# Kernel tuning notes

Measured on AMD Instinct MI355X. Metric: run time of the kernel, lower is better.

## Reference

```python
import jax, jax.numpy as jnp
import numpy as np

N = 50000      # nodes
E = 800000     # edges (avg degree 16)
IN = 128       # in_channels
HID = 64       # hidden_channels
OUT = 64       # out_channels
H = 2          # attention heads
EDIM = 16      # edge feature dim
NEG_SLOPE = 0.2


def setup_inputs() -> dict:
    key = jax.random.key(0)
    ks = jax.random.split(key, 16)
    p = lambda k, shape: (jax.random.normal(k, shape, jnp.float32) * 0.1)
    return {
        'x': jax.random.normal(ks[0], (N, IN), jnp.float32),
        'edge_index': jax.random.randint(ks[1], (2, E), 0, N, dtype=jnp.int64),
        'edge_attr': jax.random.normal(ks[2], (E, EDIM), jnp.float32),
        # GAT layer 1 (in=IN -> HID, heads=H, concat=False, edge_dim=EDIM)
        'W1': p(ks[3], (IN, H * HID)),
        'We1': p(ks[4], (EDIM, H * HID)),
        'as1': p(ks[5], (H, HID)),
        'ad1': p(ks[6], (H, HID)),
        'ae1': p(ks[7], (H, HID)),
        'b1': jnp.zeros((HID,), jnp.float32),
        # GAT layer 2 (in=HID -> OUT)
        'W2': p(ks[8], (HID, H * OUT)),
        'We2': p(ks[9], (EDIM, H * OUT)),
        'as2': p(ks[10], (H, OUT)),
        'ad2': p(ks[11], (H, OUT)),
        'ae2': p(ks[12], (H, OUT)),
        'b2': jnp.zeros((OUT,), jnp.float32),
    }


def _add_self_loops(edge_index, edge_attr, n):
    # PyG GATConv default: add_self_loops=True, fill_value='mean' ->
    # self-loop edge_attr[i] = mean of edge_attr over edges with dst == i.
    src, dst = edge_index[0], edge_index[1]
    attr_sum = jax.ops.segment_sum(edge_attr, dst, num_segments=n)          # [N, EDIM]
    cnt = jax.ops.segment_sum(jnp.ones((edge_attr.shape[0],), edge_attr.dtype), dst, num_segments=n)
    loop_attr = attr_sum / jnp.maximum(cnt, 1.0)[:, None]
    loop = jnp.arange(n, dtype=src.dtype)
    return jnp.concatenate([src, loop]), jnp.concatenate([dst, loop]), jnp.concatenate([edge_attr, loop_attr], axis=0)


def gat_layer(x, edge_index, edge_attr, W, We, att_src, att_dst, att_edge, bias, heads, out_ch):
    """PyG GATConv with edge_dim, concat=False (mean over heads)."""
    n = x.shape[0]
    src, dst, ea = _add_self_loops(edge_index, edge_attr, n)
    h = (x @ W).reshape(n, heads, out_ch)                 # [N, H, C]
    e = (ea @ We).reshape(-1, heads, out_ch)              # [E', H, C]
    a_src = jnp.sum(h * att_src, axis=-1)                 # [N, H]
    a_dst = jnp.sum(h * att_dst, axis=-1)                 # [N, H]
    a_edge = jnp.sum(e * att_edge, axis=-1)               # [E', H]
    alpha = jax.nn.leaky_relu(a_src[src] + a_dst[dst] + a_edge, NEG_SLOPE)  # [E', H]
    # segment softmax over destination node (self-loops guarantee nonempty segments)
    amax = jax.ops.segment_max(alpha, dst, num_segments=n)
    ex = jnp.exp(alpha - amax[dst])
    denom = jax.ops.segment_sum(ex, dst, num_segments=n)
    attn = ex / (denom[dst] + 1e-16)                      # [E', H]
    msg = h[src] * attn[:, :, None]                       # [E', H, C]
    out = jax.ops.segment_sum(msg, dst, num_segments=n)   # [N, H, C]
    return jnp.mean(out, axis=1) + bias, attn


def reference(x, edge_index, edge_attr, W1, We1, as1, ad1, ae1, b1, W2, We2, as2, ad2, ae2, b2):
    h1, _attn1 = gat_layer(x, edge_index, edge_attr, W1, We1, as1, ad1, ae1, b1, H, HID)
    h1 = jax.nn.relu(h1)
    h2, _attn2 = gat_layer(h1, edge_index, edge_attr, W2, We2, as2, ad2, ae2, b2, H, OUT)
    return h2
```

## Files before the change

kernel.cpp:

```cpp
#include <hip/hip_runtime.h>

#define N_NODES 50000
#define N_EDGES 800000
#define EDIM 16
#define NEG_SLOPE 0.2f

typedef _Float16 f16x8 __attribute__((ext_vector_type(8)));
typedef _Float16 f16x4 __attribute__((ext_vector_type(4)));
typedef _Float16 f16x2 __attribute__((ext_vector_type(2)));
typedef float f32x4 __attribute__((ext_vector_type(4)));

__global__ void count_rank_kernel(const int* __restrict__ ei, int* __restrict__ cnt,
                                  int* __restrict__ rank) {
    int e = blockIdx.x * blockDim.x + threadIdx.x;
    if (e < N_EDGES) rank[e] = atomicAdd(&cnt[ei[N_EDGES + e]], 1);
}

__global__ void scan_block_kernel(const int* __restrict__ in, int* __restrict__ excl,
                                  int* __restrict__ bsums, int n) {
    __shared__ int sh[256];
    int tid = threadIdx.x;
    int gid = blockIdx.x * 256 + tid;
    int v = (gid < n) ? in[gid] : 0;
    sh[tid] = v;
    __syncthreads();
    for (int off = 1; off < 256; off <<= 1) {
        int t = (tid >= off) ? sh[tid - off] : 0;
        __syncthreads();
        sh[tid] += t;
        __syncthreads();
    }
    if (gid < n) excl[gid] = sh[tid] - v;
    if (bsums != nullptr && tid == 255) bsums[blockIdx.x] = sh[tid];
}

__global__ void scan_add_kernel(const int* __restrict__ excl, const int* __restrict__ bs2,
                                int* __restrict__ csr_off, int n, int total) {
    int gid = blockIdx.x * 256 + threadIdx.x;
    if (gid < n) csr_off[gid] = excl[gid] + bs2[gid >> 8];
    if (gid == 0) csr_off[n] = total;
}

__global__ void we2_kernel(const float* __restrict__ We1, const float* __restrict__ ae1,
                           const float* __restrict__ We2, const float* __restrict__ ae2,
                           float* __restrict__ w_e) {
    int idx = threadIdx.x;
    if (idx >= 64) return;
    const float* We = (idx < 32) ? We1 : We2;
    const float* ae = (idx < 32) ? ae1 : ae2;
    int i = idx & 31;
    int h = i >> 4, d = i & 15;
    float s = 0.f;
    for (int c = 0; c < 64; ++c) s += We[d * 128 + h * 64 + c] * ae[h * 64 + c];
    w_e[idx] = s;
}

__global__ void scatter_pack_kernel(const int* __restrict__ ei, const float* __restrict__ edge_attr,
                                    const float* __restrict__ w_e, const int* __restrict__ csr_off,
                                    const int* __restrict__ rank, uint4* __restrict__ recs) {
    int e = blockIdx.x * blockDim.x + threadIdx.x;
    if (e >= N_EDGES) return;
    int s = ei[e];
    int d = ei[N_EDGES + e];
    const float* ea = edge_attr + (size_t)e * 16;
    float4 dd = make_float4(0.f, 0.f, 0.f, 0.f);
#pragma unroll
    for (int q = 0; q < 4; ++q) {
        float4 v = *reinterpret_cast<const float4*>(ea + q * 4);
        float4 wa = *reinterpret_cast<const float4*>(w_e + q * 4);
        float4 wb = *reinterpret_cast<const float4*>(w_e + 16 + q * 4);
        float4 wc = *reinterpret_cast<const float4*>(w_e + 32 + q * 4);
        float4 wd = *reinterpret_cast<const float4*>(w_e + 48 + q * 4);
        dd.x += v.x * wa.x + v.y * wa.y + v.z * wa.z + v.w * wa.w;
        dd.y += v.x * wb.x + v.y * wb.y + v.z * wb.z + v.w * wb.w;
        dd.z += v.x * wc.x + v.y * wc.y + v.z * wc.z + v.w * wc.w;
        dd.w += v.x * wd.x + v.y * wd.y + v.z * wd.z + v.w * wd.w;
    }
    f16x2 p1 = {(_Float16)dd.x, (_Float16)dd.y};
    f16x2 p2 = {(_Float16)dd.z, (_Float16)dd.w};
    int pos = csr_off[d] + rank[e];
    uint4 rec;
    rec.x = (unsigned)s;
    rec.y = __builtin_bit_cast(unsigned int, p1);
    rec.z = __builtin_bit_cast(unsigned int, p2);
    rec.w = 0u;
    recs[pos] = rec;
}

template <int K, bool F16IN>
__global__ __launch_bounds__(256) void gemm_att_kernel(const void* __restrict__ Xv,
                                                       const float* __restrict__ W,
                                                       const float* __restrict__ as_,
                                                       const float* __restrict__ ad_,
                                                       _Float16* __restrict__ H16,
                                                       float2* __restrict__ a_src,
                                                       float2* __restrict__ a_dst, int M) {
    constexpr int NCH = K / 32;
    __shared__ _Float16 wlds[8 * NCH * 64 * 8];
    const int tid = threadIdx.x;

    for (int idx = tid; idx < K * 128; idx += 256) {
        int k = idx >> 7, c = idx & 127;
        int ct = c >> 4, cl = c & 15;
        int chunk = k >> 5, grp = (k >> 3) & 3, j = k & 7;
        wlds[(((ct * NCH) + chunk) * 64 + (grp * 16 + cl)) * 8 + j] = (_Float16)W[idx];
    }
    __syncthreads();

    const int wv = tid >> 6, lane = tid & 63;
    const int lcol = lane & 15, lgrp = lane >> 4;
    const int row0 = blockIdx.x * 64 + wv * 16;
    int arow = row0 + lcol;
    if (arow >= M) arow = M - 1;

    f32x4 acc[8];
#pragma unroll
    for (int ct = 0; ct < 8; ++ct) acc[ct] = (f32x4){0.f, 0.f, 0.f, 0.f};

#pragma unroll
    for (int chunk = 0; chunk < NCH; ++chunk) {
        f16x8 afrag;
        if constexpr (F16IN) {
            const _Float16* aptr = (const _Float16*)Xv + (size_t)arow * K + lgrp * 8;
            afrag = *reinterpret_cast<const f16x8*>(aptr + chunk * 32);
        } else {
            const float* aptr = (const float*)Xv + (size_t)arow * K + lgrp * 8;
            float4 va = *reinterpret_cast<const float4*>(aptr + chunk * 32);
            float4 vb = *reinterpret_cast<const float4*>(aptr + chunk * 32 + 4);
            afrag = (f16x8){(_Float16)va.x, (_Float16)va.y, (_Float16)va.z, (_Float16)va.w,
                            (_Float16)vb.x, (_Float16)vb.y, (_Float16)vb.z, (_Float16)vb.w};
        }
#pragma unroll
        for (int ct = 0; ct < 8; ++ct) {
            f16x8 bfrag = *reinterpret_cast<const f16x8*>(&wlds[((ct * NCH + chunk) * 64 + lane) * 8]);
            acc[ct] = __builtin_amdgcn_mfma_f32_16x16x32_f16(afrag, bfrag, acc[ct], 0, 0, 0);
        }
    }

    float asv[8], adv[8];
#pragma unroll
    for (int ct = 0; ct < 8; ++ct) {
        asv[ct] = as_[ct * 16 + lcol];
        adv[ct] = ad_[ct * 16 + lcol];
    }

#pragma unroll
    for (int r = 0; r < 4; ++r) {
        int grow = row0 + lgrp * 4 + r;
        float s0 = 0.f, s1 = 0.f, d0 = 0.f, d1 = 0.f;
#pragma unroll
        for (int ct = 0; ct < 8; ++ct) {
            float v = acc[ct][r];
            if (grow < M) H16[(size_t)grow * 128 + ct * 16 + lcol] = (_Float16)v;
            if (ct < 4) { s0 += v * asv[ct]; d0 += v * adv[ct]; }
            else        { s1 += v * asv[ct]; d1 += v * adv[ct]; }
        }
#pragma unroll
        for (int m = 1; m < 16; m <<= 1) {
            s0 += __shfl_xor(s0, m);
            s1 += __shfl_xor(s1, m);
            d0 += __shfl_xor(d0, m);
            d1 += __shfl_xor(d1, m);
        }
        if (lcol == 0 && grow < M) {
            a_src[grow] = make_float2(s0, s1);
            a_dst[grow] = make_float2(d0, d1);
        }
    }
}

#define AGG_STAGE(PREG, II)                                                        \
    do {                                                                           \
        int sl_ = 2 * (II) + sub;                                                  \
        float e0b_ = __shfl(ex0, sl_);                                             \
        float e1b_ = __shfl(ex1, sl_);                                             \
        float exu_ = h1sel ? e1b_ : e0b_;                                          \
        int svn_ = __shfl(sv, (sl_ + 4) & 63);                                     \
        acc0 = fmaf(exu_, (float)PREG.x, acc0);                                    \
        acc1 = fmaf(exu_, (float)PREG.y, acc1);                                    \
        acc2 = fmaf(exu_, (float)PREG.z, acc2);                                    \
        acc3 = fmaf(exu_, (float)PREG.w, acc3);                                    \
        PREG = *reinterpret_cast<const f16x4*>(hb + ((size_t)(unsigned)svn_ << 8)); \
    } while (0)

__global__ void aggregate_kernel(const int* __restrict__ csr_off, const uint4* __restrict__ recs,
                                 const float2* __restrict__ a_src, const float2* __restrict__ a_dst,
                                 const _Float16* __restrict__ H16, const float* __restrict__ bias,
                                 float* __restrict__ out32, _Float16* __restrict__ out16,
                                 int layer, int do_relu) {
    int wid = (blockIdx.x * blockDim.x + threadIdx.x) >> 6;
    int lane = threadIdx.x & 63;
    if (wid >= N_NODES) return;
    const int n = wid;
    const int q = lane & 31;
    const int sub = lane >> 5;
    const bool h1sel = q >= 16;
    const char* hb = reinterpret_cast<const char*>(H16) + q * 8;

    float2 adn = a_dst[n];
    float2 asn = a_src[n];
    int b = csr_off[n], e = csr_off[n + 1];

    float acc0 = 0.f, acc1 = 0.f, acc2 = 0.f, acc3 = 0.f;
    float den0 = 0.f, den1 = 0.f;
    float sae0 = 0.f, sae1 = 0.f;

    for (int base = b; base < e; base += 64) {
        int j = base + lane;
        bool act = j < e;
        int sv = n;
        float ex0 = 0.f, ex1 = 0.f;
        if (act) {
            uint4 rec = recs[j];
            sv = (int)rec.x;
            unsigned aeu = layer ? rec.z : rec.y;
            f16x2 aev = __builtin_bit_cast(f16x2, aeu);
            float ael0 = (float)aev.x, ael1 = (float)aev.y;
            sae0 += ael0;
            sae1 += ael1;
            float2 asv = a_src[sv];
            float q0 = asv.x + adn.x + ael0;
            float q1 = asv.y + adn.y + ael1;
            q0 = (q0 > 0.f) ? q0 : NEG_SLOPE * q0;
            q1 = (q1 > 0.f) ? q1 : NEG_SLOPE * q1;
            ex0 = __expf(q0);
            ex1 = __expf(q1);
        }
        float d0 = ex0, d1 = ex1;
#pragma unroll
        for (int m = 32; m; m >>= 1) {
            d0 += __shfl_xor(d0, m);
            d1 += __shfl_xor(d1, m);
        }
        den0 += d0;
        den1 += d1;

        int m = e - base;
        if (m > 64) m = 64;
        int nit = (m + 1) >> 1;
        f16x4 pA, pB;
        int s0_ = __shfl(sv, sub);
        pA = *reinterpret_cast<const f16x4*>(hb + ((size_t)(unsigned)s0_ << 8));
        int s1_ = __shfl(sv, 2 + sub);
        pB = *reinterpret_cast<const f16x4*>(hb + ((size_t)(unsigned)s1_ << 8));
        for (int i = 0; i < nit; i += 2) {
            AGG_STAGE(pA, i);
            AGG_STAGE(pB, i + 1);
        }
    }

    acc0 += __shfl_xor(acc0, 32);
    acc1 += __shfl_xor(acc1, 32);
    acc2 += __shfl_xor(acc2, 32);
    acc3 += __shfl_xor(acc3, 32);

#pragma unroll
    for (int m = 32; m; m >>= 1) {
        sae0 += __shfl_xor(sae0, m);
        sae1 += __shfl_xor(sae1, m);
    }
    int deg = e - b;
    float invd = (deg > 0) ? (1.f / (float)deg) : 0.f;
    float l0 = asn.x + adn.x + sae0 * invd;
    float l1 = asn.y + adn.y + sae1 * invd;
    l0 = (l0 > 0.f) ? l0 : NEG_SLOPE * l0;
    l1 = (l1 > 0.f) ? l1 : NEG_SLOPE * l1;
    float exs0 = __expf(l0), exs1 = __expf(l1);
    den0 += exs0;
    den1 += exs1;
    float exsu = h1sel ? exs1 : exs0;
    f16x4 hs = *reinterpret_cast<const f16x4*>(hb + ((size_t)(unsigned)n << 8));
    acc0 = fmaf(exsu, (float)hs.x, acc0);
    acc1 = fmaf(exsu, (float)hs.y, acc1);
    acc2 = fmaf(exsu, (float)hs.z, acc2);
    acc3 = fmaf(exsu, (float)hs.w, acc3);

    float invden = 1.f / ((h1sel ? den1 : den0) + 1e-16f);
    float r0 = acc0 * invden;
    float r1 = acc1 * invden;
    float r2 = acc2 * invden;
    float r3 = acc3 * invden;
    float t0 = __shfl_xor(r0, 16);
    float t1 = __shfl_xor(r1, 16);
    float t2 = __shfl_xor(r2, 16);
    float t3 = __shfl_xor(r3, 16);
    if (lane < 16) {
        float4 bv = *reinterpret_cast<const float4*>(bias + q * 4);
        float o0 = 0.5f * (r0 + t0) + bv.x;
        float o1 = 0.5f * (r1 + t1) + bv.y;
        float o2 = 0.5f * (r2 + t2) + bv.z;
        float o3 = 0.5f * (r3 + t3) + bv.w;
        if (do_relu) {
            o0 = fmaxf(o0, 0.f); o1 = fmaxf(o1, 0.f);
            o2 = fmaxf(o2, 0.f); o3 = fmaxf(o3, 0.f);
        }
        if (out32) {
            float4 ov = {o0, o1, o2, o3};
            *reinterpret_cast<float4*>(out32 + (size_t)n * 64 + q * 4) = ov;
        }
        if (out16) {
            f16x4 ov16 = {(_Float16)o0, (_Float16)o1, (_Float16)o2, (_Float16)o3};
            *reinterpret_cast<f16x4*>(out16 + (size_t)n * 64 + q * 4) = ov16;
        }
    }
}

extern "C" void kernel_launch(void* const* d_in, const int* in_sizes, int n_in,
                              void* d_out, int out_size, void* d_ws, size_t ws_size,
                              hipStream_t stream) {
    const float* x = (const float*)d_in[0];
    const int* ei = (const int*)d_in[1];
    const float* edge_attr = (const float*)d_in[2];
    const float* W1 = (const float*)d_in[3];
    const float* We1 = (const float*)d_in[4];
    const float* as1 = (const float*)d_in[5];
    const float* ad1 = (const float*)d_in[6];
    const float* ae1 = (const float*)d_in[7];
    const float* b1 = (const float*)d_in[8];
    const float* W2 = (const float*)d_in[9];
    const float* We2 = (const float*)d_in[10];
    const float* as2 = (const float*)d_in[11];
    const float* ad2 = (const float*)d_in[12];
    const float* ae2 = (const float*)d_in[13];
    const float* b2 = (const float*)d_in[14];
    float* out = (float*)d_out;

    char* ws = (char*)d_ws;
    size_t off = 0;
    auto alloc = [&](size_t bytes) -> void* {
        void* p = ws + off;
        off += (bytes + 255) & ~(size_t)255;
        return p;
    };
    int* cnt = (int*)alloc((size_t)N_NODES * 4);
    int* csr_off = (int*)alloc(((size_t)N_NODES + 1) * 4);
    int* rank = (int*)alloc((size_t)N_EDGES * 4);
    int* excl = (int*)alloc((size_t)N_NODES * 4);
    int* bsums = (int*)alloc(256 * 4);
    int* bsums2 = (int*)alloc(256 * 4);
    uint4* recs = (uint4*)alloc((size_t)N_EDGES * 16);
    _Float16* H16 = (_Float16*)alloc((size_t)N_NODES * 128 * 2);
    _Float16* h1_16 = (_Float16*)alloc((size_t)N_NODES * 64 * 2);
    float* a_src = (float*)alloc((size_t)N_NODES * 2 * 4);
    float* a_dst = (float*)alloc((size_t)N_NODES * 2 * 4);
    float* w_e = (float*)alloc(64 * 4);

    const int nb = (N_NODES + 255) / 256;
    const int eb = (N_EDGES + 255) / 256;

    hipMemsetAsync(cnt, 0, (size_t)N_NODES * 4, stream);
    we2_kernel<<<1, 64, 0, stream>>>(We1, ae1, We2, ae2, w_e);
    count_rank_kernel<<<eb, 256, 0, stream>>>(ei, cnt, rank);
    scan_block_kernel<<<nb, 256, 0, stream>>>(cnt, excl, bsums, N_NODES);
    scan_block_kernel<<<1, 256, 0, stream>>>(bsums, bsums2, nullptr, nb);
    scan_add_kernel<<<nb, 256, 0, stream>>>(excl, bsums2, csr_off, N_NODES, N_EDGES);
    scatter_pack_kernel<<<eb, 256, 0, stream>>>(ei, edge_attr, w_e, csr_off, rank, recs);

    const int nodeWaveBlocks = (N_NODES * 64 + 255) / 256;
    const int gemmBlocks = (N_NODES + 63) / 64;

    gemm_att_kernel<128, false><<<gemmBlocks, 256, 0, stream>>>(x, W1, as1, ad1, H16,
                                                                (float2*)a_src, (float2*)a_dst, N_NODES);
    aggregate_kernel<<<nodeWaveBlocks, 256, 0, stream>>>(csr_off, recs,
                                                         (const float2*)a_src, (const float2*)a_dst,
                                                         H16, b1, nullptr, h1_16, 0, 1);

    gemm_att_kernel<64, true><<<gemmBlocks, 256, 0, stream>>>(h1_16, W2, as2, ad2, H16,
                                                              (float2*)a_src, (float2*)a_dst, N_NODES);
    aggregate_kernel<<<nodeWaveBlocks, 256, 0, stream>>>(csr_off, recs,
                                                         (const float2*)a_src, (const float2*)a_dst,
                                                         H16, b2, out, nullptr, 1, 0);
}
```

Before: 188.3 us.

## Gather 16-byte neighbor rows with four edges per wave step in aggregation

Restructures the aggregation kernel so each lane loads 8 half values (16 bytes) instead of 4. The wave now processes four source edges per step instead of two, with a three-deep register prefetch pipeline instead of two. Tail edges are masked by zeroing the weight, since a step can now run past the valid edge count. This should halve the number of loop iterations and issue wider gather loads per edge, at the cost of more accumulator registers and an extra cross-lane reduction at the end.

```diff
diff --git a/kernel.cpp b/kernel.cpp
--- a/kernel.cpp
+++ b/kernel.cpp
@@ -171,16 +171,21 @@
 
 #define AGG_STAGE(PREG, II)                                                        \
     do {                                                                           \
-        int sl_ = 2 * (II) + sub;                                                  \
+        int sl_ = 4 * (II) + sub;                                                  \
         float e0b_ = __shfl(ex0, sl_);                                             \
         float e1b_ = __shfl(ex1, sl_);                                             \
         float exu_ = h1sel ? e1b_ : e0b_;                                          \
-        int svn_ = __shfl(sv, (sl_ + 4) & 63);                                     \
-        acc0 = fmaf(exu_, (float)PREG.x, acc0);                                    \
-        acc1 = fmaf(exu_, (float)PREG.y, acc1);                                    \
-        acc2 = fmaf(exu_, (float)PREG.z, acc2);                                    \
-        acc3 = fmaf(exu_, (float)PREG.w, acc3);                                    \
-        PREG = *reinterpret_cast<const f16x4*>(hb + ((size_t)(unsigned)svn_ << 8)); \
+        exu_ = (sl_ < m) ? exu_ : 0.f;                                             \
+        int svn_ = __shfl(sv, (sl_ + 12) & 63);                                    \
+        acc0 = fmaf(exu_, (float)PREG[0], acc0);                                   \
+        acc1 = fmaf(exu_, (float)PREG[1], acc1);                                   \
+        acc2 = fmaf(exu_, (float)PREG[2], acc2);                                   \
+        acc3 = fmaf(exu_, (float)PREG[3], acc3);                                   \
+        acc4 = fmaf(exu_, (float)PREG[4], acc4);                                   \
+        acc5 = fmaf(exu_, (float)PREG[5], acc5);                                   \
+        acc6 = fmaf(exu_, (float)PREG[6], acc6);                                   \
+        acc7 = fmaf(exu_, (float)PREG[7], acc7);                                   \
+        PREG = *reinterpret_cast<const f16x8*>(hb + ((size_t)(unsigned)svn_ << 8)); \
     } while (0)
 
 __global__ void aggregate_kernel(const int* __restrict__ csr_off, const uint4* __restrict__ recs,
@@ -192,16 +197,17 @@
     int lane = threadIdx.x & 63;
     if (wid >= N_NODES) return;
     const int n = wid;
-    const int q = lane & 31;
-    const int sub = lane >> 5;
-    const bool h1sel = q >= 16;
-    const char* hb = reinterpret_cast<const char*>(H16) + q * 8;
+    const int r = lane & 15;
+    const int sub = lane >> 4;
+    const bool h1sel = r >= 8;
+    const char* hb = reinterpret_cast<const char*>(H16) + r * 16;
 
     float2 adn = a_dst[n];
     float2 asn = a_src[n];
     int b = csr_off[n], e = csr_off[n + 1];
 
     float acc0 = 0.f, acc1 = 0.f, acc2 = 0.f, acc3 = 0.f;
+    float acc4 = 0.f, acc5 = 0.f, acc6 = 0.f, acc7 = 0.f;
     float den0 = 0.f, den1 = 0.f;
     float sae0 = 0.f, sae1 = 0.f;
 
@@ -228,36 +234,41 @@
         }
         float d0 = ex0, d1 = ex1;
 #pragma unroll
-        for (int m = 32; m; m >>= 1) {
-            d0 += __shfl_xor(d0, m);
-            d1 += __shfl_xor(d1, m);
+        for (int m2 = 32; m2; m2 >>= 1) {
+            d0 += __shfl_xor(d0, m2);
+            d1 += __shfl_xor(d1, m2);
         }
         den0 += d0;
         den1 += d1;
 
         int m = e - base;
         if (m > 64) m = 64;
-        int nit = (m + 1) >> 1;
-        f16x4 pA, pB;
-        int s0_ = __shfl(sv, sub);
-        pA = *reinterpret_cast<const f16x4*>(hb + ((size_t)(unsigned)s0_ << 8));
-        int s1_ = __shfl(sv, 2 + sub);
-        pB = *reinterpret_cast<const f16x4*>(hb + ((size_t)(unsigned)s1_ << 8));
-        for (int i = 0; i < nit; i += 2) {
+        int nst = (m + 3) >> 2;
+        f16x8 pA, pB, pC;
+        int s_;
+        s_ = __shfl(sv, sub);     pA = *reinterpret_cast<const f16x8*>(hb + ((size_t)(unsigned)s_ << 8));
+        s_ = __shfl(sv, 4 + sub); pB = *reinterpret_cast<const f16x8*>(hb + ((size_t)(unsigned)s_ << 8));
+        s_ = __shfl(sv, 8 + sub); pC = *reinterpret_cast<const f16x8*>(hb + ((size_t)(unsigned)s_ << 8));
+        for (int i = 0; i < nst; i += 3) {
             AGG_STAGE(pA, i);
             AGG_STAGE(pB, i + 1);
-        }
-    }
-
-    acc0 += __shfl_xor(acc0, 32);
-    acc1 += __shfl_xor(acc1, 32);
-    acc2 += __shfl_xor(acc2, 32);
-    acc3 += __shfl_xor(acc3, 32);
-
-#pragma unroll
-    for (int m = 32; m; m >>= 1) {
-        sae0 += __shfl_xor(sae0, m);
-        sae1 += __shfl_xor(sae1, m);
+            AGG_STAGE(pC, i + 2);
+        }
+    }
+
+    acc0 += __shfl_xor(acc0, 16); acc1 += __shfl_xor(acc1, 16);
+    acc2 += __shfl_xor(acc2, 16); acc3 += __shfl_xor(acc3, 16);
+    acc4 += __shfl_xor(acc4, 16); acc5 += __shfl_xor(acc5, 16);
+    acc6 += __shfl_xor(acc6, 16); acc7 += __shfl_xor(acc7, 16);
+    acc0 += __shfl_xor(acc0, 32); acc1 += __shfl_xor(acc1, 32);
+    acc2 += __shfl_xor(acc2, 32); acc3 += __shfl_xor(acc3, 32);
+    acc4 += __shfl_xor(acc4, 32); acc5 += __shfl_xor(acc5, 32);
+    acc6 += __shfl_xor(acc6, 32); acc7 += __shfl_xor(acc7, 32);
+
+#pragma unroll
+    for (int m2 = 32; m2; m2 >>= 1) {
+        sae0 += __shfl_xor(sae0, m2);
+        sae1 += __shfl_xor(sae1, m2);
     }
     int deg = e - b;
     float invd = (deg > 0) ? (1.f / (float)deg) : 0.f;
@@ -269,38 +280,48 @@
     den0 += exs0;
     den1 += exs1;
     float exsu = h1sel ? exs1 : exs0;
-    f16x4 hs = *reinterpret_cast<const f16x4*>(hb + ((size_t)(unsigned)n << 8));
-    acc0 = fmaf(exsu, (float)hs.x, acc0);
-    acc1 = fmaf(exsu, (float)hs.y, acc1);
-    acc2 = fmaf(exsu, (float)hs.z, acc2);
-    acc3 = fmaf(exsu, (float)hs.w, acc3);
+    f16x8 hs = *reinterpret_cast<const f16x8*>(hb + ((size_t)(unsigned)n << 8));
+    acc0 = fmaf(exsu, (float)hs[0], acc0);
+    acc1 = fmaf(exsu, (float)hs[1], acc1);
+    acc2 = fmaf(exsu, (float)hs[2], acc2);
+    acc3 = fmaf(exsu, (float)hs[3], acc3);
+    acc4 = fmaf(exsu, (float)hs[4], acc4);
+    acc5 = fmaf(exsu, (float)hs[5], acc5);
+    acc6 = fmaf(exsu, (float)hs[6], acc6);
+    acc7 = fmaf(exsu, (float)hs[7], acc7);
 
     float invden = 1.f / ((h1sel ? den1 : den0) + 1e-16f);
-    float r0 = acc0 * invden;
-    float r1 = acc1 * invden;
-    float r2 = acc2 * invden;
-    float r3 = acc3 * invden;
-    float t0 = __shfl_xor(r0, 16);
-    float t1 = __shfl_xor(r1, 16);
-    float t2 = __shfl_xor(r2, 16);
-    float t3 = __shfl_xor(r3, 16);
-    if (lane < 16) {
-        float4 bv = *reinterpret_cast<const float4*>(bias + q * 4);
-        float o0 = 0.5f * (r0 + t0) + bv.x;
-        float o1 = 0.5f * (r1 + t1) + bv.y;
-        float o2 = 0.5f * (r2 + t2) + bv.z;
-        float o3 = 0.5f * (r3 + t3) + bv.w;
+    float r0 = acc0 * invden, r1 = acc1 * invden, r2 = acc2 * invden, r3 = acc3 * invden;
+    float r4 = acc4 * invden, r5 = acc5 * invden, r6 = acc6 * invden, r7 = acc7 * invden;
+    float t0 = __shfl_xor(r0, 8), t1 = __shfl_xor(r1, 8);
+    float t2 = __shfl_xor(r2, 8), t3 = __shfl_xor(r3, 8);
+    float t4 = __shfl_xor(r4, 8), t5 = __shfl_xor(r5, 8);
+    float t6 = __shfl_xor(r6, 8), t7 = __shfl_xor(r7, 8);
+    if (lane < 8) {
+        float4 bva = *reinterpret_cast<const float4*>(bias + r * 8);
+        float4 bvb = *reinterpret_cast<const float4*>(bias + r * 8 + 4);
+        float o0 = 0.5f * (r0 + t0) + bva.x;
+        float o1 = 0.5f * (r1 + t1) + bva.y;
+        float o2 = 0.5f * (r2 + t2) + bva.z;
+        float o3 = 0.5f * (r3 + t3) + bva.w;
+        float o4 = 0.5f * (r4 + t4) + bvb.x;
+        float o5 = 0.5f * (r5 + t5) + bvb.y;
+        float o6 = 0.5f * (r6 + t6) + bvb.z;
+        float o7 = 0.5f * (r7 + t7) + bvb.w;
         if (do_relu) {
-            o0 = fmaxf(o0, 0.f); o1 = fmaxf(o1, 0.f);
-            o2 = fmaxf(o2, 0.f); o3 = fmaxf(o3, 0.f);
+            o0 = fmaxf(o0, 0.f); o1 = fmaxf(o1, 0.f); o2 = fmaxf(o2, 0.f); o3 = fmaxf(o3, 0.f);
+            o4 = fmaxf(o4, 0.f); o5 = fmaxf(o5, 0.f); o6 = fmaxf(o6, 0.f); o7 = fmaxf(o7, 0.f);
         }
         if (out32) {
-            float4 ov = {o0, o1, o2, o3};
-            *reinterpret_cast<float4*>(out32 + (size_t)n * 64 + q * 4) = ov;
+            float4 ova = {o0, o1, o2, o3};
+            float4 ovb = {o4, o5, o6, o7};
+            *reinterpret_cast<float4*>(out32 + (size_t)n * 64 + r * 8) = ova;
+            *reinterpret_cast<float4*>(out32 + (size_t)n * 64 + r * 8 + 4) = ovb;
         }
         if (out16) {
-            f16x4 ov16 = {(_Float16)o0, (_Float16)o1, (_Float16)o2, (_Float16)o3};
-            *reinterpret_cast<f16x4*>(out16 + (size_t)n * 64 + q * 4) = ov16;
+            f16x8 ov16 = {(_Float16)o0, (_Float16)o1, (_Float16)o2, (_Float16)o3,
+                          (_Float16)o4, (_Float16)o5, (_Float16)o6, (_Float16)o7};
+            *reinterpret_cast<f16x8*>(out16 + (size_t)n * 64 + r * 8) = ov16;
         }
     }
 }
```

After: 203.2 us. 7.9% more time.
